# Kernel optimization log

Measured on AMD Instinct MI355X. Metric: run time of the kernel, lower is better.

Reference implementation:

```python
import jax, jax.numpy as jnp
import numpy as np

B, N, C, D = 4, 8192, 3, 128


def chamfer_loss(x, y):
    # x: [B,N,3], y: [B,M,3]. Squared-distance chamfer with min-NN both ways.
    x2 = jnp.sum(x * x, axis=-1)                      # [B,N]
    y2 = jnp.sum(y * y, axis=-1)                      # [B,M]
    xy = jnp.einsum('bnc,bmc->bnm', x, y)             # [B,N,M] -- dominant 1GB buffer
    d2 = x2[:, :, None] + y2[:, None, :] - 2.0 * xy
    return jnp.mean(jnp.min(d2, axis=2)) + jnp.mean(jnp.min(d2, axis=1))


def setup_inputs() -> dict:
    key = jax.random.key(0)
    k1, k2, k3, k4 = jax.random.split(key, 4)
    return {
        'encoder_input': jax.random.normal(k1, (B, N, C), jnp.float32),
        'decoder_input': jax.random.normal(k2, (B, N, C), jnp.float32),
        'W1': jax.random.normal(k3, (C, D), jnp.float32) * 0.1,
        'b1': jnp.zeros((D,), jnp.float32),
        'W2': jax.random.normal(k4, (2 * D, C), jnp.float32) * 0.01,
        'b2': jnp.zeros((C,), jnp.float32),
    }


def reference(encoder_input, decoder_input, W1, b1, W2, b2):
    # Point-wise embedding (stand-in for the black-box DGCNN encoder)
    f_e = jax.nn.relu(encoder_input @ W1 + b1)        # [B,N,D]
    f_d = jax.nn.relu(decoder_input @ W1 + b1)        # [B,N,D]
    # Cross-set mixing (stand-in for transformer(embed_in, embed_out)),
    # concatenated with the decoder 'global_feat' as in the original.
    cross = f_d + jnp.mean(f_e, axis=1, keepdims=True)
    feat = jnp.concatenate([cross, f_d], axis=-1)     # [B,N,2D]
    displacement = feat @ W2 + b2                     # [B,N,3]
    warped = displacement + decoder_input             # warped = disp + decoder xyz
    loss1 = chamfer_loss(encoder_input, warped)       # all-pairs NN chamfer (the kernel target)
    return warped, loss1
```

## Files before the change

### kernel.cpp

```cpp
#include <hip/hip_runtime.h>
#include <hip/hip_bf16.h>
#include <hip/hip_fp16.h>
#include <float.h>

#define BB 4
#define NN 8192
#define DD 128

typedef __attribute__((ext_vector_type(8))) _Float16 f16x8;
typedef __attribute__((ext_vector_type(16))) float f32x16;
typedef __attribute__((ext_vector_type(4))) unsigned int u32x4;

__device__ __forceinline__ unsigned int pk2h(float a, float b) {
    __half2 h = __floats2half2_rn(a, b);
    return *reinterpret_cast<unsigned int*>(&h);
}


__global__ void mean_fe_kernel(const float* __restrict__ enc,
                               const float* __restrict__ W1,
                               const float* __restrict__ b1,
                               float* __restrict__ meanEp) {
    __shared__ float pts[256 * 3];
    __shared__ float red[256];
    int bid = blockIdx.x;
    int bt = bid >> 5;
    int chunk = bid & 31;
    int tid = threadIdx.x;
    int k = tid & 127;
    int half = tid >> 7;
    int base = (bt * NN + chunk * 256) * 3;
    for (int i = tid; i < 768; i += 256) pts[i] = enc[base + i];
    float w0 = W1[k], w1 = W1[128 + k], w2 = W1[256 + k], bk = b1[k];
    __syncthreads();
    float acc = 0.f;
    int p0 = half * 128;
#pragma unroll 4
    for (int i = 0; i < 128; ++i) {
        int p = (p0 + i) * 3;
        float v = pts[p] * w0 + pts[p + 1] * w1 + pts[p + 2] * w2 + bk;
        acc += fmaxf(v, 0.f);
    }
    red[tid] = acc;
    __syncthreads();
    if (tid < 128) meanEp[bid * 128 + k] = red[tid] + red[tid + 128];
}

__global__ void warp_kernel(const float* __restrict__ dec,
                            const float* __restrict__ W1,
                            const float* __restrict__ b1,
                            const float* __restrict__ W2,
                            const float* __restrict__ b2,
                            const float* __restrict__ meanEp,
                            unsigned int* __restrict__ buf,
                            float* __restrict__ out,
                            float* __restrict__ loss_slot) {
    __shared__ float sW1[384];
    __shared__ float sb1[128];
    __shared__ float sW2[768];
    __shared__ float sME[128];
    int tid = threadIdx.x;
    int idx = blockIdx.x * 256 + tid;
    int bt = idx >> 13;
    for (int i = tid; i < 384; i += 256) sW1[i] = W1[i];
    for (int i = tid; i < 768; i += 256) sW2[i] = W2[i];
    if (tid < 128) {
        sb1[tid] = b1[tid];
        float s = 0.f;
#pragma unroll 8
        for (int c = 0; c < 32; ++c) s += meanEp[(bt * 32 + c) * 128 + tid];
        sME[tid] = s;
    }
    buf[idx] = 0x7F7FFFFFu;
    buf[32768 + idx] = 0x7F7FFFFFu;
    if (idx == 0) *loss_slot = 0.f;
    __syncthreads();
    float d0 = dec[idx * 3], d1 = dec[idx * 3 + 1], d2 = dec[idx * 3 + 2];
    float a0 = 0.f, a1 = 0.f, a2 = 0.f;
    float m0 = 0.f, m1 = 0.f, m2 = 0.f;
#pragma unroll 4
    for (int k = 0; k < 128; ++k) {
        float fd = fmaxf(d0 * sW1[k] + d1 * sW1[128 + k] + d2 * sW1[256 + k] + sb1[k], 0.f);
        float wl0 = sW2[k * 3], wl1 = sW2[k * 3 + 1], wl2 = sW2[k * 3 + 2];
        float wh0 = sW2[(128 + k) * 3], wh1 = sW2[(128 + k) * 3 + 1], wh2 = sW2[(128 + k) * 3 + 2];
        a0 += fd * (wl0 + wh0);
        a1 += fd * (wl1 + wh1);
        a2 += fd * (wl2 + wh2);
        float me = sME[k];
        m0 += me * wl0; m1 += me * wl1; m2 += me * wl2;
    }
    const float invN = 1.0f / NN;
    out[idx * 3]     = a0 + m0 * invN + b2[0] + d0;
    out[idx * 3 + 1] = a1 + m1 * invN + b2[1] + d1;
    out[idx * 3 + 2] = a2 + m2 * invN + b2[2] + d2;
}

__device__ __forceinline__ float tree16(const f32x16& p) {
    float t0 = fminf(fminf(p[0], p[1]), p[2]);
    float t1 = fminf(fminf(p[3], p[4]), p[5]);
    float t2 = fminf(fminf(p[6], p[7]), p[8]);
    float t3 = fminf(fminf(p[9], p[10]), p[11]);
    float t4 = fminf(fminf(p[12], p[13]), p[14]);
    float r0 = fminf(fminf(t0, t1), p[15]);
    float r1 = fminf(fminf(t2, t3), t4);
    return fminf(r0, r1);
}

__global__ __launch_bounds__(256, 4) void chamfer_mfma_kernel(
        const float* __restrict__ enc,
        const float* __restrict__ warped,
        unsigned int* __restrict__ buf) {
    __shared__ __align__(16) union {
        unsigned int syb[1024 * 4 + 4];
        float rmin[128 * 33];
    } sh;
    __shared__ float colminW[4][1024];

    int bid = blockIdx.x;
    int bt = bid >> 9;
    int xc = (bid >> 3) & 63;
    int ys = bid & 7;
    int tid = threadIdx.x;
    int lane = tid & 63, wave = tid >> 6;

    int ybase = bt * NN + ys * 1024;
#pragma unroll
    for (int i = 0; i < 4; ++i) {
        int p = tid + i * 256;
        int g = (ybase + p) * 3;
        float y0 = warped[g], y1 = warped[g + 1], y2 = warped[g + 2];
        float w = y0 * y0 + y1 * y1 + y2 * y2;
        u32x4 v = { pk2h(y0, y1), pk2h(y2, 1.f), pk2h(w, 1.f), 0u };
        *reinterpret_cast<u32x4*>(&sh.syb[p * 4]) = v;
    }
    if (tid < 4) sh.syb[4096 + tid] = 0u;

    f16x8 afrag = {};
    int xbase = bt * NN + xc * 128 + wave * 32;
    if (lane < 32) {
        int g = (xbase + lane) * 3;
        float a = enc[g], c = enc[g + 1], e = enc[g + 2];
        float s = a * a + c * c + e * e;
        afrag[0] = (_Float16)(-2.f * a);
        afrag[1] = (_Float16)(-2.f * c);
        afrag[2] = (_Float16)(-2.f * e);
        afrag[3] = (_Float16)s;
        afrag[4] = (_Float16)1.f;
        afrag[5] = (_Float16)1.f;
    }
    __syncthreads();

    const char* base = (const char*)sh.syb + ((lane < 32) ? lane * 16 : 16384);
    int str = (lane < 32) ? 512 : 0;

    float racc[16];
#pragma unroll
    for (int i = 0; i < 16; ++i) racc[i] = FLT_MAX;
    f32x16 zero = {};

    f16x8 bC = *(const f16x8*)(base);
    f16x8 bD = *(const f16x8*)(base + str);
    f32x16 qa = __builtin_amdgcn_mfma_f32_32x32x16_f16(afrag, bC, zero, 0, 0, 0);
    f32x16 qb = __builtin_amdgcn_mfma_f32_32x32x16_f16(afrag, bD, zero, 0, 0, 0);
    bC = *(const f16x8*)(base + 2 * str);
    bD = *(const f16x8*)(base + 3 * str);

#pragma unroll
    for (int t = 0; t < 16; ++t) {
        f32x16 pa = qa, pb = qb;
        if (t < 15) {
            qa = __builtin_amdgcn_mfma_f32_32x32x16_f16(afrag, bC, zero, 0, 0, 0);
            qb = __builtin_amdgcn_mfma_f32_32x32x16_f16(afrag, bD, zero, 0, 0, 0);
        }
        if (t < 14) {
            bC = *(const f16x8*)(base + (2 * t + 4) * str);
            bD = *(const f16x8*)(base + (2 * t + 5) * str);
        }
#pragma unroll
        for (int i = 0; i < 16; ++i)
            racc[i] = fminf(racc[i], fminf(pa[i], pb[i]));
        float ca = tree16(pa);
        float cb = tree16(pb);
        ca = fminf(ca, __shfl_xor(ca, 32));
        cb = fminf(cb, __shfl_xor(cb, 32));
        float sel = (lane < 32) ? ca : cb;
        colminW[wave][t * 64 + lane] = sel;
    }

    __syncthreads();

    int col = lane & 31, half = lane >> 5;
#pragma unroll
    for (int i = 0; i < 16; ++i) {
        int row = wave * 32 + (i & 3) + 8 * (i >> 2) + 4 * half;
        sh.rmin[row * 33 + col] = racc[i];
    }
#pragma unroll
    for (int i = 0; i < 4; ++i) {
        int p = tid + i * 256;
        float m = fminf(fminf(colminW[0][p], colminW[1][p]),
                        fminf(colminW[2][p], colminW[3][p]));
        atomicMin(&buf[32768 + bt * NN + ys * 1024 + p], __float_as_uint(m));
    }
    __syncthreads();
    if (tid < 128) {
        float m = sh.rmin[tid * 33];
#pragma unroll
        for (int j = 1; j < 32; ++j) m = fminf(m, sh.rmin[tid * 33 + j]);
        atomicMin(&buf[bt * NN + xc * 128 + tid], __float_as_uint(m));
    }
}

__global__ void reduce_loss_kernel(const unsigned int* __restrict__ buf,
                                   float* __restrict__ loss_slot) {
    __shared__ float red[256];
    int tid = threadIdx.x;
    int idx = blockIdx.x * 256 + tid;
    float s = 0.f;
#pragma unroll
    for (int i = 0; i < 4; ++i)
        s += __uint_as_float(buf[idx + i * 16384]);
    red[tid] = s;
    __syncthreads();
    for (int off = 128; off > 0; off >>= 1) {
        if (tid < off) red[tid] += red[tid + off];
        __syncthreads();
    }
    if (tid == 0) {
        float v = red[0] * (1.0f / (BB * NN));
        if (blockIdx.x == 0) v -= 2.0f;
        atomicAdd(loss_slot, v);
    }
}

extern "C" void kernel_launch(void* const* d_in, const int* in_sizes, int n_in,
                              void* d_out, int out_size, void* d_ws, size_t ws_size,
                              hipStream_t stream) {
    const float* enc = (const float*)d_in[0];
    const float* dec = (const float*)d_in[1];
    const float* W1  = (const float*)d_in[2];
    const float* b1  = (const float*)d_in[3];
    const float* W2  = (const float*)d_in[4];
    const float* b2  = (const float*)d_in[5];
    float* out = (float*)d_out;

    unsigned int* buf = (unsigned int*)d_ws;
    float* meanEp = (float*)((char*)d_ws + 262144);
    float* loss_slot = out + BB * NN * 3;

    mean_fe_kernel<<<BB * 32, 256, 0, stream>>>(enc, W1, b1, meanEp);
    warp_kernel<<<BB * NN / 256, 256, 0, stream>>>(dec, W1, b1, W2, b2, meanEp,
                                                   buf, out, loss_slot);
    chamfer_mfma_kernel<<<BB * 64 * 8, 256, 0, stream>>>(enc, out, buf);
    reduce_loss_kernel<<<64, 256, 0, stream>>>(buf, loss_slot);
}
```

Baseline: 47.35 us.

## Replace global atomicMin with per-block partial minima reduced in final kernel

The chamfer kernel now writes per-block row and column minima to dedicated partial buffers instead of issuing global atomicMin into a shared buffer. The reduction kernel then takes the min across the 8 y-slices and 64 x-chunks before summing. This removes atomic contention and the buffer initialisation in the warp kernel. In exchange it adds about 8 MB of partial writes and strided reads in the reduction, which now runs 128 blocks.

After: 60.84 us. 28.5% more time.

```diff
diff --git a/kernel.cpp b/kernel.cpp
--- a/kernel.cpp
+++ b/kernel.cpp
@@ -52,7 +52,6 @@
                             const float* __restrict__ W2,
                             const float* __restrict__ b2,
                             const float* __restrict__ meanEp,
-                            unsigned int* __restrict__ buf,
                             float* __restrict__ out,
                             float* __restrict__ loss_slot) {
     __shared__ float sW1[384];
@@ -71,8 +70,6 @@
         for (int c = 0; c < 32; ++c) s += meanEp[(bt * 32 + c) * 128 + tid];
         sME[tid] = s;
     }
-    buf[idx] = 0x7F7FFFFFu;
-    buf[32768 + idx] = 0x7F7FFFFFu;
     if (idx == 0) *loss_slot = 0.f;
     __syncthreads();
     float d0 = dec[idx * 3], d1 = dec[idx * 3 + 1], d2 = dec[idx * 3 + 2];
@@ -109,7 +106,8 @@
 __global__ __launch_bounds__(256, 4) void chamfer_mfma_kernel(
         const float* __restrict__ enc,
         const float* __restrict__ warped,
-        unsigned int* __restrict__ buf) {
+        float* __restrict__ rowpart,
+        float* __restrict__ colpart) {
     __shared__ __align__(16) union {
         unsigned int syb[1024 * 4 + 4];
         float rmin[128 * 33];
@@ -189,38 +187,50 @@
 
     __syncthreads();
 
-    int col = lane & 31, half = lane >> 5;
-#pragma unroll
-    for (int i = 0; i < 16; ++i) {
-        int row = wave * 32 + (i & 3) + 8 * (i >> 2) + 4 * half;
-        sh.rmin[row * 33 + col] = racc[i];
-    }
 #pragma unroll
     for (int i = 0; i < 4; ++i) {
         int p = tid + i * 256;
         float m = fminf(fminf(colminW[0][p], colminW[1][p]),
                         fminf(colminW[2][p], colminW[3][p]));
-        atomicMin(&buf[32768 + bt * NN + ys * 1024 + p], __float_as_uint(m));
+        colpart[bid * 1024 + p] = m;
+    }
+
+    int col = lane & 31, half = lane >> 5;
+#pragma unroll
+    for (int i = 0; i < 16; ++i) {
+        int row = wave * 32 + (i & 3) + 8 * (i >> 2) + 4 * half;
+        sh.rmin[row * 33 + col] = racc[i];
     }
     __syncthreads();
     if (tid < 128) {
         float m = sh.rmin[tid * 33];
 #pragma unroll
         for (int j = 1; j < 32; ++j) m = fminf(m, sh.rmin[tid * 33 + j]);
-        atomicMin(&buf[bt * NN + xc * 128 + tid], __float_as_uint(m));
-    }
-}
-
-__global__ void reduce_loss_kernel(const unsigned int* __restrict__ buf,
+        rowpart[bid * 128 + tid] = m;
+    }
+}
+
+__global__ void reduce_loss_kernel(const float* __restrict__ rowpart,
+                                   const float* __restrict__ colpart,
                                    float* __restrict__ loss_slot) {
     __shared__ float red[256];
     int tid = threadIdx.x;
-    int idx = blockIdx.x * 256 + tid;
-    float s = 0.f;
-#pragma unroll
-    for (int i = 0; i < 4; ++i)
-        s += __uint_as_float(buf[idx + i * 16384]);
-    red[tid] = s;
+    int g = blockIdx.x * 256 + tid;
+    int bt = g >> 13, rem = g & 8191;
+
+    int xc = rem >> 7, r = rem & 127;
+    const float* rp = rowpart + (bt * 512 + xc * 8) * 128 + r;
+    float rm = rp[0];
+#pragma unroll
+    for (int ys = 1; ys < 8; ++ys) rm = fminf(rm, rp[ys * 128]);
+
+    int ys = rem >> 10, p = rem & 1023;
+    const float* cp = colpart + (bt * 512 + ys) * 1024 + p;
+    float cm = cp[0];
+#pragma unroll 8
+    for (int x = 1; x < 64; ++x) cm = fminf(cm, cp[x * 8 * 1024]);
+
+    red[tid] = rm + cm;
     __syncthreads();
     for (int off = 128; off > 0; off >>= 1) {
         if (tid < off) red[tid] += red[tid + off];
@@ -244,13 +254,14 @@
     const float* b2  = (const float*)d_in[5];
     float* out = (float*)d_out;
 
-    unsigned int* buf = (unsigned int*)d_ws;
-    float* meanEp = (float*)((char*)d_ws + 262144);
+    float* rowpart = (float*)d_ws;
+    float* colpart = (float*)((char*)d_ws + (1u << 20));
+    float* meanEp  = (float*)((char*)d_ws + (9u << 20));
     float* loss_slot = out + BB * NN * 3;
 
     mean_fe_kernel<<<BB * 32, 256, 0, stream>>>(enc, W1, b1, meanEp);
     warp_kernel<<<BB * NN / 256, 256, 0, stream>>>(dec, W1, b1, W2, b2, meanEp,
-                                                   buf, out, loss_slot);
-    chamfer_mfma_kernel<<<BB * 64 * 8, 256, 0, stream>>>(enc, out, buf);
-    reduce_loss_kernel<<<64, 256, 0, stream>>>(buf, loss_slot);
-}
+                                                   out, loss_slot);
+    chamfer_mfma_kernel<<<BB * 64 * 8, 256, 0, stream>>>(enc, out, rowpart, colpart);
+    reduce_loss_kernel<<<128, 256, 0, stream>>>(rowpart, colpart, loss_slot);
+}
```

## Fuse loss reduction into chamfer kernel via last-blocks ticket counter

Applied to the files above, without the earlier changes.

Removes the separate reduce_loss launch. Each chamfer block takes a ticket from a global atomic counter, and the last 64 blocks to finish sum the per-point min buffer. They read it through atomicMin so the values are coherent. The MFMA loop also drops its two-deep accumulator software pipeline for a simpler one-step operand prefetch, and the row-min spill is moved after the column atomics. The fused reduction depends on the last 64 tickets seeing every earlier block's atomics, which adds ordering risk, and the tail blocks lengthen the kernel's end.

Result: slower. 62.59 us (+32.2%).

```diff
diff --git a/kernel.cpp b/kernel.cpp
--- a/kernel.cpp
+++ b/kernel.cpp
@@ -53,6 +53,7 @@
                             const float* __restrict__ b2,
                             const float* __restrict__ meanEp,
                             unsigned int* __restrict__ buf,
+                            unsigned int* __restrict__ counter,
                             float* __restrict__ out,
                             float* __restrict__ loss_slot) {
     __shared__ float sW1[384];
@@ -73,7 +74,7 @@
     }
     buf[idx] = 0x7F7FFFFFu;
     buf[32768 + idx] = 0x7F7FFFFFu;
-    if (idx == 0) *loss_slot = 0.f;
+    if (idx == 0) { *loss_slot = 0.f; *counter = 0u; }
     __syncthreads();
     float d0 = dec[idx * 3], d1 = dec[idx * 3 + 1], d2 = dec[idx * 3 + 2];
     float a0 = 0.f, a1 = 0.f, a2 = 0.f;
@@ -106,15 +107,21 @@
     return fminf(r0, r1);
 }
 
+#define NBLK 2048
+#define NRED 64
+
 __global__ __launch_bounds__(256, 4) void chamfer_mfma_kernel(
         const float* __restrict__ enc,
         const float* __restrict__ warped,
-        unsigned int* __restrict__ buf) {
+        unsigned int* __restrict__ buf,
+        unsigned int* __restrict__ counter,
+        float* __restrict__ loss_slot) {
     __shared__ __align__(16) union {
         unsigned int syb[1024 * 4 + 4];
         float rmin[128 * 33];
     } sh;
     __shared__ float colminW[4][1024];
+    __shared__ unsigned int ticket_s;
 
     int bid = blockIdx.x;
     int bt = bid >> 9;
@@ -158,43 +165,31 @@
     for (int i = 0; i < 16; ++i) racc[i] = FLT_MAX;
     f32x16 zero = {};
 
-    f16x8 bC = *(const f16x8*)(base);
-    f16x8 bD = *(const f16x8*)(base + str);
-    f32x16 qa = __builtin_amdgcn_mfma_f32_32x32x16_f16(afrag, bC, zero, 0, 0, 0);
-    f32x16 qb = __builtin_amdgcn_mfma_f32_32x32x16_f16(afrag, bD, zero, 0, 0, 0);
-    bC = *(const f16x8*)(base + 2 * str);
-    bD = *(const f16x8*)(base + 3 * str);
-
+    f16x8 b0 = *(const f16x8*)(base);
+    f16x8 b1 = *(const f16x8*)(base + str);
 #pragma unroll
     for (int t = 0; t < 16; ++t) {
-        f32x16 pa = qa, pb = qb;
+        f16x8 n0 = b0, n1 = b1;
         if (t < 15) {
-            qa = __builtin_amdgcn_mfma_f32_32x32x16_f16(afrag, bC, zero, 0, 0, 0);
-            qb = __builtin_amdgcn_mfma_f32_32x32x16_f16(afrag, bD, zero, 0, 0, 0);
+            n0 = *(const f16x8*)(base + (2 * t + 2) * str);
+            n1 = *(const f16x8*)(base + (2 * t + 3) * str);
         }
-        if (t < 14) {
-            bC = *(const f16x8*)(base + (2 * t + 4) * str);
-            bD = *(const f16x8*)(base + (2 * t + 5) * str);
-        }
+        f32x16 q0 = __builtin_amdgcn_mfma_f32_32x32x16_f16(afrag, b0, zero, 0, 0, 0);
+        f32x16 q1 = __builtin_amdgcn_mfma_f32_32x32x16_f16(afrag, b1, zero, 0, 0, 0);
 #pragma unroll
         for (int i = 0; i < 16; ++i)
-            racc[i] = fminf(racc[i], fminf(pa[i], pb[i]));
-        float ca = tree16(pa);
-        float cb = tree16(pb);
+            racc[i] = fminf(racc[i], fminf(q0[i], q1[i]));
+        float ca = tree16(q0);
+        float cb = tree16(q1);
         ca = fminf(ca, __shfl_xor(ca, 32));
         cb = fminf(cb, __shfl_xor(cb, 32));
         float sel = (lane < 32) ? ca : cb;
         colminW[wave][t * 64 + lane] = sel;
-    }
-
-    __syncthreads();
-
-    int col = lane & 31, half = lane >> 5;
-#pragma unroll
-    for (int i = 0; i < 16; ++i) {
-        int row = wave * 32 + (i & 3) + 8 * (i >> 2) + 4 * half;
-        sh.rmin[row * 33 + col] = racc[i];
-    }
+        b0 = n0; b1 = n1;
+    }
+
+    __syncthreads();
+
 #pragma unroll
     for (int i = 0; i < 4; ++i) {
         int p = tid + i * 256;
@@ -202,6 +197,12 @@
                         fminf(colminW[2][p], colminW[3][p]));
         atomicMin(&buf[32768 + bt * NN + ys * 1024 + p], __float_as_uint(m));
     }
+    int col = lane & 31, half = lane >> 5;
+#pragma unroll
+    for (int i = 0; i < 16; ++i) {
+        int row = wave * 32 + (i & 3) + 8 * (i >> 2) + 4 * half;
+        sh.rmin[row * 33 + col] = racc[i];
+    }
     __syncthreads();
     if (tid < 128) {
         float m = sh.rmin[tid * 33];
@@ -209,26 +210,31 @@
         for (int j = 1; j < 32; ++j) m = fminf(m, sh.rmin[tid * 33 + j]);
         atomicMin(&buf[bt * NN + xc * 128 + tid], __float_as_uint(m));
     }
-}
-
-__global__ void reduce_loss_kernel(const unsigned int* __restrict__ buf,
-                                   float* __restrict__ loss_slot) {
-    __shared__ float red[256];
-    int tid = threadIdx.x;
-    int idx = blockIdx.x * 256 + tid;
+
+    __syncthreads();
+    if (tid == 0)
+        ticket_s = __hip_atomic_fetch_add(counter, 1u, __ATOMIC_ACQ_REL,
+                                          __HIP_MEMORY_SCOPE_AGENT);
+    __syncthreads();
+    unsigned int ticket = ticket_s;
+    if (ticket < NBLK - NRED) return;
+
+    int r = ticket - (NBLK - NRED);
     float s = 0.f;
 #pragma unroll
-    for (int i = 0; i < 4; ++i)
-        s += __uint_as_float(buf[idx + i * 16384]);
-    red[tid] = s;
+    for (int i = 0; i < 4; ++i) {
+        int p = r * 1024 + tid + i * 256;
+        s += __uint_as_float(atomicMin(&buf[p], 0x7F7FFFFFu));
+    }
+    colminW[0][tid] = s;
     __syncthreads();
     for (int off = 128; off > 0; off >>= 1) {
-        if (tid < off) red[tid] += red[tid + off];
+        if (tid < off) colminW[0][tid] += colminW[0][tid + off];
         __syncthreads();
     }
     if (tid == 0) {
-        float v = red[0] * (1.0f / (BB * NN));
-        if (blockIdx.x == 0) v -= 2.0f;
+        float v = colminW[0][0] * (1.0f / (BB * NN));
+        if (r == 0) v -= 2.0f;
         atomicAdd(loss_slot, v);
     }
 }
@@ -245,12 +251,12 @@
     float* out = (float*)d_out;
 
     unsigned int* buf = (unsigned int*)d_ws;
-    float* meanEp = (float*)((char*)d_ws + 262144);
+    unsigned int* counter = (unsigned int*)((char*)d_ws + 262144);
+    float* meanEp = (float*)((char*)d_ws + 262656);
     float* loss_slot = out + BB * NN * 3;
 
     mean_fe_kernel<<<BB * 32, 256, 0, stream>>>(enc, W1, b1, meanEp);
     warp_kernel<<<BB * NN / 256, 256, 0, stream>>>(dec, W1, b1, W2, b2, meanEp,
-                                                   buf, out, loss_slot);
-    chamfer_mfma_kernel<<<BB * 64 * 8, 256, 0, stream>>>(enc, out, buf);
-    reduce_loss_kernel<<<64, 256, 0, stream>>>(buf, loss_slot);
-}
+                                                   buf, counter, out, loss_slot);
+    chamfer_mfma_kernel<<<NBLK, 256, 0, stream>>>(enc, out, buf, counter, loss_slot);
+}
```

## Precompute fp16 B-fragments in warp kernel and enlarge chamfer tiles with two-stage staging

Applied to the files above, without the earlier changes.

The warp kernel now writes pre-packed fp16 MFMA B-fragments (xyz, squared norm, ones) to workspace, so the chamfer kernel no longer recomputes them from the warped floats. The chamfer kernel moves to 512-thread blocks covering 256 x-points by 2048 y-points in two 1024-point LDS stages, which cuts the grid from 2048 to 512 blocks. Column minima go through shared atomicMin per stage. Row minima are reduced in-wave with shuffles and written as per-y-group partials, which removes the global row atomics. The reduce kernel takes the min over the four partials. This trades fewer redundant y loads and atomics for fewer blocks and more LDS atomic traffic.

New measurement: 50.64 us. 6.9% more time.

```diff
diff --git a/kernel.cpp b/kernel.cpp
--- a/kernel.cpp
+++ b/kernel.cpp
@@ -52,7 +52,8 @@
                             const float* __restrict__ W2,
                             const float* __restrict__ b2,
                             const float* __restrict__ meanEp,
-                            unsigned int* __restrict__ buf,
+                            u32x4* __restrict__ bfragbuf,
+                            unsigned int* __restrict__ colbuf,
                             float* __restrict__ out,
                             float* __restrict__ loss_slot) {
     __shared__ float sW1[384];
@@ -71,8 +72,7 @@
         for (int c = 0; c < 32; ++c) s += meanEp[(bt * 32 + c) * 128 + tid];
         sME[tid] = s;
     }
-    buf[idx] = 0x7F7FFFFFu;
-    buf[32768 + idx] = 0x7F7FFFFFu;
+    colbuf[idx] = 0x7F7FFFFFu;
     if (idx == 0) *loss_slot = 0.f;
     __syncthreads();
     float d0 = dec[idx * 3], d1 = dec[idx * 3 + 1], d2 = dec[idx * 3 + 2];
@@ -90,9 +90,15 @@
         m0 += me * wl0; m1 += me * wl1; m2 += me * wl2;
     }
     const float invN = 1.0f / NN;
-    out[idx * 3]     = a0 + m0 * invN + b2[0] + d0;
-    out[idx * 3 + 1] = a1 + m1 * invN + b2[1] + d1;
-    out[idx * 3 + 2] = a2 + m2 * invN + b2[2] + d2;
+    float o0 = a0 + m0 * invN + b2[0] + d0;
+    float o1 = a1 + m1 * invN + b2[1] + d1;
+    float o2 = a2 + m2 * invN + b2[2] + d2;
+    out[idx * 3]     = o0;
+    out[idx * 3 + 1] = o1;
+    out[idx * 3 + 2] = o2;
+    float w = o0 * o0 + o1 * o1 + o2 * o2;
+    u32x4 v = { pk2h(o0, o1), pk2h(o2, 1.f), pk2h(w, 1.f), 0u };
+    bfragbuf[idx] = v;
 }
 
 __device__ __forceinline__ float tree16(const f32x16& p) {
@@ -106,37 +112,34 @@
     return fminf(r0, r1);
 }
 
-__global__ __launch_bounds__(256, 4) void chamfer_mfma_kernel(
+__global__ __launch_bounds__(512, 4) void chamfer_mfma_kernel(
         const float* __restrict__ enc,
-        const float* __restrict__ warped,
-        unsigned int* __restrict__ buf) {
-    __shared__ __align__(16) union {
-        unsigned int syb[1024 * 4 + 4];
-        float rmin[128 * 33];
-    } sh;
-    __shared__ float colminW[4][1024];
+        const u32x4* __restrict__ bfragbuf,
+        unsigned int* __restrict__ colbuf,
+        float* __restrict__ rowpart) {
+    __shared__ __align__(16) unsigned int syb[2][4100];
+    __shared__ unsigned int colmin[2][1024];
 
     int bid = blockIdx.x;
-    int bt = bid >> 9;
-    int xc = (bid >> 3) & 63;
-    int ys = bid & 7;
+    int bt = bid >> 7;
+    int xc = (bid >> 2) & 31;
+    int yg = bid & 3;
     int tid = threadIdx.x;
     int lane = tid & 63, wave = tid >> 6;
 
-    int ybase = bt * NN + ys * 1024;
-#pragma unroll
-    for (int i = 0; i < 4; ++i) {
-        int p = tid + i * 256;
-        int g = (ybase + p) * 3;
-        float y0 = warped[g], y1 = warped[g + 1], y2 = warped[g + 2];
-        float w = y0 * y0 + y1 * y1 + y2 * y2;
-        u32x4 v = { pk2h(y0, y1), pk2h(y2, 1.f), pk2h(w, 1.f), 0u };
-        *reinterpret_cast<u32x4*>(&sh.syb[p * 4]) = v;
-    }
-    if (tid < 4) sh.syb[4096 + tid] = 0u;
+    int ybase = bt * NN + yg * 2048;
+    u32x4 v0 = bfragbuf[ybase + tid];
+    u32x4 v1 = bfragbuf[ybase + 512 + tid];
+    u32x4 v2 = bfragbuf[ybase + 1024 + tid];
+    u32x4 v3 = bfragbuf[ybase + 1536 + tid];
+
+#pragma unroll
+    for (int i = 0; i < 4; ++i)
+        ((unsigned int*)colmin)[tid + i * 512] = 0x7F7FFFFFu;
+    if (tid < 8) syb[tid >> 2][4096 + (tid & 3)] = 0u;
 
     f16x8 afrag = {};
-    int xbase = bt * NN + xc * 128 + wave * 32;
+    int xbase = bt * NN + xc * 256 + wave * 32;
     if (lane < 32) {
         int g = (xbase + lane) * 3;
         float a = enc[g], c = enc[g + 1], e = enc[g + 2];
@@ -148,79 +151,77 @@
         afrag[4] = (_Float16)1.f;
         afrag[5] = (_Float16)1.f;
     }
-    __syncthreads();
-
-    const char* base = (const char*)sh.syb + ((lane < 32) ? lane * 16 : 16384);
-    int str = (lane < 32) ? 512 : 0;
+
+    *reinterpret_cast<u32x4*>(&syb[0][tid * 4]) = v0;
+    *reinterpret_cast<u32x4*>(&syb[0][(tid + 512) * 4]) = v1;
 
     float racc[16];
 #pragma unroll
     for (int i = 0; i < 16; ++i) racc[i] = FLT_MAX;
     f32x16 zero = {};
 
-    f16x8 bC = *(const f16x8*)(base);
-    f16x8 bD = *(const f16x8*)(base + str);
-    f32x16 qa = __builtin_amdgcn_mfma_f32_32x32x16_f16(afrag, bC, zero, 0, 0, 0);
-    f32x16 qb = __builtin_amdgcn_mfma_f32_32x32x16_f16(afrag, bD, zero, 0, 0, 0);
-    bC = *(const f16x8*)(base + 2 * str);
-    bD = *(const f16x8*)(base + 3 * str);
-
-#pragma unroll
-    for (int t = 0; t < 16; ++t) {
-        f32x16 pa = qa, pb = qb;
-        if (t < 15) {
-            qa = __builtin_amdgcn_mfma_f32_32x32x16_f16(afrag, bC, zero, 0, 0, 0);
-            qb = __builtin_amdgcn_mfma_f32_32x32x16_f16(afrag, bD, zero, 0, 0, 0);
+    const char* base0 = (const char*)(&syb[0][0]) + ((lane < 32) ? lane * 16 : 16384);
+    const char* base1 = (const char*)(&syb[1][0]) + ((lane < 32) ? lane * 16 : 16384);
+    int str = (lane < 32) ? 512 : 0;
+
+    auto compute = [&](const char* base, int ch) {
+#pragma unroll
+        for (int t = 0; t < 16; ++t) {
+            f16x8 b0 = *(const f16x8*)(base + (2 * t) * str);
+            f16x8 b1 = *(const f16x8*)(base + (2 * t + 1) * str);
+            f32x16 q0 = __builtin_amdgcn_mfma_f32_32x32x16_f16(afrag, b0, zero, 0, 0, 0);
+            f32x16 q1 = __builtin_amdgcn_mfma_f32_32x32x16_f16(afrag, b1, zero, 0, 0, 0);
+#pragma unroll
+            for (int i = 0; i < 16; ++i)
+                racc[i] = fminf(racc[i], fminf(q0[i], q1[i]));
+            float ca = tree16(q0);
+            float cb = tree16(q1);
+            ca = fminf(ca, __shfl_xor(ca, 32));
+            cb = fminf(cb, __shfl_xor(cb, 32));
+            float sel = (lane < 32) ? ca : cb;
+            atomicMin(&colmin[ch][t * 64 + lane], __float_as_uint(sel));
         }
-        if (t < 14) {
-            bC = *(const f16x8*)(base + (2 * t + 4) * str);
-            bD = *(const f16x8*)(base + (2 * t + 5) * str);
-        }
+    };
+
+    __syncthreads();
+    compute(base0, 0);
+    *reinterpret_cast<u32x4*>(&syb[1][tid * 4]) = v2;
+    *reinterpret_cast<u32x4*>(&syb[1][(tid + 512) * 4]) = v3;
+    __syncthreads();
+    atomicMin(&colbuf[ybase + tid], colmin[0][tid]);
+    atomicMin(&colbuf[ybase + tid + 512], colmin[0][tid + 512]);
+    compute(base1, 1);
+    __syncthreads();
+    atomicMin(&colbuf[ybase + 1024 + tid], colmin[1][tid]);
+    atomicMin(&colbuf[ybase + 1536 + tid], colmin[1][tid + 512]);
+
+#pragma unroll
+    for (int s = 1; s <= 16; s <<= 1) {
 #pragma unroll
         for (int i = 0; i < 16; ++i)
-            racc[i] = fminf(racc[i], fminf(pa[i], pb[i]));
-        float ca = tree16(pa);
-        float cb = tree16(pb);
-        ca = fminf(ca, __shfl_xor(ca, 32));
-        cb = fminf(cb, __shfl_xor(cb, 32));
-        float sel = (lane < 32) ? ca : cb;
-        colminW[wave][t * 64 + lane] = sel;
-    }
-
-    __syncthreads();
-
-    int col = lane & 31, half = lane >> 5;
-#pragma unroll
-    for (int i = 0; i < 16; ++i) {
-        int row = wave * 32 + (i & 3) + 8 * (i >> 2) + 4 * half;
-        sh.rmin[row * 33 + col] = racc[i];
-    }
-#pragma unroll
-    for (int i = 0; i < 4; ++i) {
-        int p = tid + i * 256;
-        float m = fminf(fminf(colminW[0][p], colminW[1][p]),
-                        fminf(colminW[2][p], colminW[3][p]));
-        atomicMin(&buf[32768 + bt * NN + ys * 1024 + p], __float_as_uint(m));
-    }
-    __syncthreads();
-    if (tid < 128) {
-        float m = sh.rmin[tid * 33];
-#pragma unroll
-        for (int j = 1; j < 32; ++j) m = fminf(m, sh.rmin[tid * 33 + j]);
-        atomicMin(&buf[bt * NN + xc * 128 + tid], __float_as_uint(m));
-    }
-}
-
-__global__ void reduce_loss_kernel(const unsigned int* __restrict__ buf,
+            racc[i] = fminf(racc[i], __shfl_xor(racc[i], s));
+    }
+    if ((lane & 31) == 0) {
+        int hi = lane >> 5;
+        float* rp = rowpart + yg * (BB * NN) + bt * NN + xc * 256 + wave * 32 + 4 * hi;
+#pragma unroll
+        for (int i = 0; i < 16; ++i)
+            rp[(i & 3) + 8 * (i >> 2)] = racc[i];
+    }
+}
+
+__global__ void reduce_loss_kernel(const float* __restrict__ rowpart,
+                                   const unsigned int* __restrict__ colbuf,
                                    float* __restrict__ loss_slot) {
     __shared__ float red[256];
     int tid = threadIdx.x;
-    int idx = blockIdx.x * 256 + tid;
-    float s = 0.f;
-#pragma unroll
-    for (int i = 0; i < 4; ++i)
-        s += __uint_as_float(buf[idx + i * 16384]);
-    red[tid] = s;
+    int g = blockIdx.x * 256 + tid;
+    float rm = rowpart[g];
+#pragma unroll
+    for (int ygi = 1; ygi < 4; ++ygi)
+        rm = fminf(rm, rowpart[ygi * (BB * NN) + g]);
+    float cm = __uint_as_float(colbuf[g]);
+    red[tid] = rm + cm;
     __syncthreads();
     for (int off = 128; off > 0; off >>= 1) {
         if (tid < off) red[tid] += red[tid + off];
@@ -244,13 +245,15 @@
     const float* b2  = (const float*)d_in[5];
     float* out = (float*)d_out;
 
-    unsigned int* buf = (unsigned int*)d_ws;
-    float* meanEp = (float*)((char*)d_ws + 262144);
+    u32x4* bfragbuf = (u32x4*)d_ws;
+    unsigned int* colbuf = (unsigned int*)((char*)d_ws + (512u << 10));
+    float* rowpart = (float*)((char*)d_ws + (640u << 10));
+    float* meanEp  = (float*)((char*)d_ws + (1152u << 10));
     float* loss_slot = out + BB * NN * 3;
 
     mean_fe_kernel<<<BB * 32, 256, 0, stream>>>(enc, W1, b1, meanEp);
     warp_kernel<<<BB * NN / 256, 256, 0, stream>>>(dec, W1, b1, W2, b2, meanEp,
-                                                   buf, out, loss_slot);
-    chamfer_mfma_kernel<<<BB * 64 * 8, 256, 0, stream>>>(enc, out, buf);
-    reduce_loss_kernel<<<64, 256, 0, stream>>>(buf, loss_slot);
-}
+                                                   bfragbuf, colbuf, out, loss_slot);
+    chamfer_mfma_kernel<<<512, 512, 0, stream>>>(enc, bfragbuf, colbuf, rowpart);
+    reduce_loss_kernel<<<128, 256, 0, stream>>>(rowpart, colbuf, loss_slot);
+}
```
